# Optimization experiments

Measured on AMD Instinct MI355X. Metric: run time of the kernel, lower is better.

The kernel has to match this reference:

```python
import jax, jax.numpy as jnp
import numpy as np
import math

B, T = 8, 1024
IN_DIMS = 1024
OUT_DIMS = 1024
NUM_CODES = 1024
NUM_CODEBOOKS = 8


def setup_inputs() -> dict:
    key = jax.random.key(0)
    k1, k2, k3, k4, k5 = jax.random.split(key, 5)
    x = jax.random.normal(k1, (B, T, IN_DIMS), dtype=jnp.float32)
    target = jax.random.randint(k2, (B, T, NUM_CODEBOOKS), 0, NUM_CODES, dtype=jnp.int64)
    # params, init per reset_params()
    codebook = jax.random.normal(k3, (NUM_CODES, NUM_CODEBOOKS, OUT_DIMS), dtype=jnp.float32) / math.sqrt(OUT_DIMS * NUM_CODEBOOKS)
    proj_w = jax.random.normal(k4, (NUM_CODEBOOKS * NUM_CODES, IN_DIMS), dtype=jnp.float32) / math.sqrt(IN_DIMS)
    proj_b = jnp.zeros((NUM_CODEBOOKS * NUM_CODES,), dtype=jnp.float32)
    wproj_w = jax.random.normal(k5, (NUM_CODEBOOKS, IN_DIMS), dtype=jnp.float32) / math.sqrt(IN_DIMS)
    return {"x": x, "target": target, "codebook": codebook,
            "proj_w": proj_w, "proj_b": proj_b, "wproj_w": wproj_w}


def reference(x, target, codebook, proj_w, proj_b, wproj_w):
    # xp: (B, T, K, C)
    xp = (jnp.einsum('btd,nd->btn', x, proj_w) + proj_b).reshape(B, T, NUM_CODEBOOKS, NUM_CODES)
    # xw: (B, T, K) softmax codebook weights
    xw = jax.nn.softmax(jnp.einsum('btd,kd->btk', x, wproj_w), axis=-1)
    # gather codebook embeddings under no_grad: codebook[target, arange(K)] -> (B, T, K, D)
    cb_inds = jnp.arange(NUM_CODEBOOKS)
    codebook_embs = jax.lax.stop_gradient(codebook[target, cb_inds])
    # per-element cross entropy, reduction='none' -> (B, T, K)
    logp = jax.nn.log_softmax(xp, axis=-1)
    x_loss = -jnp.take_along_axis(logp, target[..., None], axis=-1)[..., 0]
    # softmax-weighted sum over codebooks -> (B, T, D)
    emb = jnp.einsum('btkd,btk->btd', codebook_embs, xw)
    return emb, x_loss
```

## Files before the change

kernel.cpp:

```cpp
#include <hip/hip_runtime.h>
#include <hip/hip_bf16.h>
#include <math.h>

#define MTOT   8192
#define KDIM   1024
#define NCODES 1024
#define NCB    8
#define NTOT   8192
#define ODIM   1024

typedef __attribute__((ext_vector_type(8))) short  bf16x8;
typedef __attribute__((ext_vector_type(4))) float  f32x4;

__device__ __forceinline__ ushort f2bf(float f) {
  union { float f; unsigned u; } v; v.f = f;
  unsigned u = v.u;
  unsigned r = (u + 0x7fffu + ((u >> 16) & 1u)) >> 16;
  return (ushort)r;
}

__device__ __forceinline__ void gload16(const void* g, void* l) {
  __builtin_amdgcn_global_load_lds(
      (const __attribute__((address_space(1))) void*)g,
      (__attribute__((address_space(3))) void*)l,
      16, 0, 0);
}

__global__ void cvt_bf16_kernel(const float* __restrict__ in,
                                ushort* __restrict__ out) {
  int i = blockIdx.x * blockDim.x + threadIdx.x;
  float4 v = ((const float4*)in)[i];
  ushort4 o;
  o.x = f2bf(v.x); o.y = f2bf(v.y); o.z = f2bf(v.z); o.w = f2bf(v.w);
  ((ushort4*)out)[i] = o;
}


#define SRC_DEC(c) ((((c) >> 7) * 16 + (((c) >> 3) & 15)) * 2048 \
                    + ((((c) & 7) ^ (((c) >> 3) & 7)) << 4))

#define STAGE(T) do { \
    const int kt_ = (T) & 15, ns_ = (T) >> 4, P_ = (T) & 1; \
    const char* as_ = Ag + kt_ * 128; \
    char* ad_ = ldsA_st + P_ * 32768; \
    gload16(as_ + srcA0, ad_); \
    gload16(as_ + srcA1, ad_ + 8192); \
    gload16(as_ + srcA2, ad_ + 16384); \
    gload16(as_ + srcA3, ad_ + 24576); \
    const char* bs_ = Bg + ns_ * 262144 + kt_ * 128; \
    char* bd_ = ldsB_st + P_ * 16384; \
    gload16(bs_ + srcA0, bd_); \
    gload16(bs_ + srcA1, bd_ + 8192); \
  } while(0)

#define READS(T, AR, BR) do { \
    const int P_ = (T) & 1; \
    const char* ab_ = ldsA_rd + P_ * 32768; \
    const char* bb_ = ldsB_rd + P_ * 16384; \
    _Pragma("unroll") for (int m_ = 0; m_ < 4; ++m_) { \
      AR[m_][0] = *(const bf16x8*)(ab_ + m_ * 2048 + ik0); \
      AR[m_][1] = *(const bf16x8*)(ab_ + m_ * 2048 + ik1); \
    } \
    _Pragma("unroll") for (int n_ = 0; n_ < 4; ++n_) { \
      BR[n_][0] = *(const bf16x8*)(bb_ + n_ * 2048 + ik0); \
      BR[n_][1] = *(const bf16x8*)(bb_ + n_ * 2048 + ik1); \
    } \
  } while(0)

#define MMALL(AR, BR) do { \
    _Pragma("unroll") for (int k_ = 0; k_ < 2; ++k_) \
    _Pragma("unroll") for (int m_ = 0; m_ < 4; ++m_) \
    _Pragma("unroll") for (int n_ = 0; n_ < 4; ++n_) \
      acc[m_][n_] = __builtin_amdgcn_mfma_f32_16x16x32_bf16( \
          AR[m_][k_], BR[n_][k_], acc[m_][n_], 0, 0, 0); \
  } while(0)

#define BOUNDARY \
    asm volatile("s_waitcnt lgkmcnt(0)" ::: "memory"); \
    asm volatile("s_waitcnt vmcnt(0)" ::: "memory"); \
    asm volatile("s_barrier" ::: "memory");

#define FLUSH(SEG) do { \
    const int colb_ = (SEG) * 128 + wc * 64; \
    float bias_n[4]; \
    _Pragma("unroll") for (int n_ = 0; n_ < 4; ++n_) \
      bias_n[n_] = bias[kcb * 1024 + colb_ + n_ * 16 + c15]; \
    _Pragma("unroll") for (int m_ = 0; m_ < 4; ++m_) { \
      _Pragma("unroll") for (int j_ = 0; j_ < 4; ++j_) { \
        const int rl_ = wr * 64 + m_ * 16 + g * 4 + j_; \
        const int tc_ = tgtcol[rl_]; \
        float s_ = 0.f; \
        _Pragma("unroll") for (int n_ = 0; n_ < 4; ++n_) { \
          const float v_ = acc[m_][n_][j_] + bias_n[n_]; \
          if (colb_ + n_ * 16 + c15 == tc_) tgtval[rl_] = v_; \
          s_ += __expf(v_); \
        } \
        _Pragma("unroll") for (int o_ = 1; o_ < 16; o_ <<= 1) \
          s_ += __shfl_xor(s_, o_); \
        if (c15 == 0) redS[wc * 256 + rl_] = s_; \
      } \
    } \
    asm volatile("s_waitcnt lgkmcnt(0)" ::: "memory"); \
    asm volatile("s_barrier" ::: "memory"); \
    if (tid < 256) S_acc += redS[tid] + redS[tid + 256]; \
    _Pragma("unroll") for (int m_ = 0; m_ < 4; ++m_) \
      _Pragma("unroll") for (int n_ = 0; n_ < 4; ++n_) \
        acc[m_][n_] = (f32x4){0.f, 0.f, 0.f, 0.f}; \
  } while(0)

__global__ __launch_bounds__(512, 2)
void ce_gemm_kernel(const ushort* __restrict__ Abf,
                    const ushort* __restrict__ Bbf,
                    const float*  __restrict__ bias,
                    const int*    __restrict__ target,
                    float* __restrict__ xloss) {
  extern __shared__ char smem[];
  float* redS   = (float*)(smem + 98304);
  int*   tgtcol = (int*)  (smem + 100352);
  float* tgtval = (float*)(smem + 101376);

  const int tid  = threadIdx.x;
  const int wid  = tid >> 6;
  const int lane = tid & 63;
  const int wr   = wid >> 1;
  const int wc   = wid & 1;
  const int g    = lane >> 4;
  const int c15  = lane & 15;
  const int bidx  = blockIdx.x;
  const int u     = bidx >> 3;
  const int mtile = (bidx & 7) * 4 + (u & 3);
  const int kcb   = u >> 2;

  const int ik0 = c15 * 128 + ((g ^ (c15 & 7)) << 4);
  const int ik1 = ik0 ^ 64;

  const char* ldsA_rd = smem + wr * 8192;
  const char* ldsB_rd = smem + 65536 + wc * 8192;
  char* ldsA_st = smem + wid * 1024;
  char* ldsB_st = smem + 65536 + wid * 1024;

  const char* Ag = ((const char*)Abf) + (size_t)mtile * 256 * 2048;
  const char* Bg = ((const char*)Bbf) + (size_t)kcb * 1024 * 2048;

  const int srcA0 = SRC_DEC(tid);
  const int srcA1 = SRC_DEC(tid + 512);
  const int srcA2 = SRC_DEC(tid + 1024);
  const int srcA3 = SRC_DEC(tid + 1536);

  if (tid < 256)
    tgtcol[tid] = target[(size_t)(mtile * 256 + tid) * NCB + kcb];

  f32x4 acc[4][4];
#pragma unroll
  for (int m = 0; m < 4; ++m)
#pragma unroll
    for (int n = 0; n < 4; ++n)
      acc[m][n] = (f32x4){0.f, 0.f, 0.f, 0.f};

  float S_acc = 0.f;
  bf16x8 a0[4][2], b0v[4][2], a1[4][2], b1v[4][2];

  STAGE(0); STAGE(1);
  asm volatile("s_waitcnt vmcnt(0)" ::: "memory");
  __syncthreads();
  READS(0, a0, b0v);

#pragma unroll 1
  for (int di = 0; di < 63; ++di) {
    const int t = 2 * di;
    STAGE(t + 2);
    READS(t + 1, a1, b1v);
    __builtin_amdgcn_s_setprio(1);
    MMALL(a0, b0v);
    __builtin_amdgcn_s_setprio(0);
    BOUNDARY
    STAGE(t + 3);
    READS(t + 2, a0, b0v);
    __builtin_amdgcn_s_setprio(1);
    MMALL(a1, b1v);
    __builtin_amdgcn_s_setprio(0);
    BOUNDARY
    if ((di & 7) == 7) FLUSH(di >> 3);
  }
  READS(127, a1, b1v);
  __builtin_amdgcn_s_setprio(1);
  MMALL(a0, b0v);
  __builtin_amdgcn_s_setprio(0);
  BOUNDARY
  MMALL(a1, b1v);
  FLUSH(7);

  if (tid < 256) {
    const int row = mtile * 256 + tid;
    xloss[(size_t)row * NCB + kcb] = __logf(S_acc) - tgtval[tid];
  }
}

__global__ void emb_kernel(const float* __restrict__ x,
                           const int*   __restrict__ target,
                           const float* __restrict__ cb,
                           const float* __restrict__ wproj,
                           float* __restrict__ emb_out,
                           ushort* __restrict__ xbf) {
  const int bt   = blockIdx.x;
  const int tid  = threadIdx.x;
  const int lane = tid & 63;
  const int wid  = tid >> 6;

  const float4 xv = ((const float4*)(x + (size_t)bt * KDIM))[tid];
  ushort4 xo;
  xo.x = f2bf(xv.x); xo.y = f2bf(xv.y); xo.z = f2bf(xv.z); xo.w = f2bf(xv.w);
  ((ushort4*)(xbf + (size_t)bt * KDIM))[tid] = xo;

  float p[8];
#pragma unroll
  for (int k = 0; k < 8; ++k) {
    const float4 wv = ((const float4*)(wproj + k * KDIM))[tid];
    p[k] = xv.x * wv.x + xv.y * wv.y + xv.z * wv.z + xv.w * wv.w;
  }
#pragma unroll
  for (int k = 0; k < 8; ++k)
#pragma unroll
    for (int off = 32; off >= 1; off >>= 1)
      p[k] += __shfl_xor(p[k], off);

  __shared__ float lred[4][8];
  if (lane == 0) {
#pragma unroll
    for (int k = 0; k < 8; ++k) lred[wid][k] = p[k];
  }
  __syncthreads();

  float logit[8], mx = -1e30f;
#pragma unroll
  for (int k = 0; k < 8; ++k) {
    logit[k] = lred[0][k] + lred[1][k] + lred[2][k] + lred[3][k];
    mx = fmaxf(mx, logit[k]);
  }
  float w[8], den = 0.f;
#pragma unroll
  for (int k = 0; k < 8; ++k) { w[k] = __expf(logit[k] - mx); den += w[k]; }
  const float inv = 1.f / den;

  float4 acc = make_float4(0.f, 0.f, 0.f, 0.f);
#pragma unroll
  for (int k = 0; k < 8; ++k) {
    const int t = target[bt * NCB + k];
    const float4 cv = ((const float4*)(cb + ((size_t)t * NCB + k) * ODIM))[tid];
    const float wk = w[k] * inv;
    acc.x += wk * cv.x; acc.y += wk * cv.y; acc.z += wk * cv.z; acc.w += wk * cv.w;
  }
  ((float4*)(emb_out + (size_t)bt * ODIM))[tid] = acc;
}

extern "C" void kernel_launch(void* const* d_in, const int* in_sizes, int n_in,
                              void* d_out, int out_size, void* d_ws, size_t ws_size,
                              hipStream_t stream) {
  const float* x        = (const float*)d_in[0];
  const int*   target   = (const int*)  d_in[1];
  const float* codebook = (const float*)d_in[2];
  const float* proj_w   = (const float*)d_in[3];
  const float* proj_b   = (const float*)d_in[4];
  const float* wproj_w  = (const float*)d_in[5];

  float* out       = (float*)d_out;
  float* emb_out   = out;
  float* xloss_out = out + (size_t)MTOT * ODIM;

  char* ws = (char*)d_ws;
  ushort* xbf = (ushort*)ws;
  ushort* wbf = (ushort*)(ws + (size_t)16 * 1024 * 1024);

  hipFuncSetAttribute((const void*)ce_gemm_kernel,
                      hipFuncAttributeMaxDynamicSharedMemorySize, 102400);

  emb_kernel<<<MTOT, 256, 0, stream>>>(x, target, codebook, wproj_w, emb_out, xbf);
  cvt_bf16_kernel<<<(NTOT * KDIM / 4) / 256, 256, 0, stream>>>(proj_w, wbf);

  ce_gemm_kernel<<<256, 512, 102400, stream>>>(xbf, wbf, proj_b, target, xloss_out);
}
```

Baseline: 194.0 us.

## Triple-buffer LDS staging in CE GEMM with partial vmcnt waits

Switches the bf16 GEMM's global-to-LDS staging from two buffers to three, issuing loads three k-steps ahead and waiting only on the oldest stage (vmcnt(6)) before each barrier instead of draining all loads. The main loop is restructured into six-step windows so buffer indices rotate mod 3 with compile-time register ping-pong. This aims to hide global load latency behind MFMA work, at the cost of raising dynamic LDS to about 148KB per block.

After: 207.0 us. 6.7% more time.

```diff
diff --git a/kernel.cpp b/kernel.cpp
--- a/kernel.cpp
+++ b/kernel.cpp
@@ -40,7 +40,7 @@
                     + ((((c) & 7) ^ (((c) >> 3) & 7)) << 4))
 
 #define STAGE(T) do { \
-    const int kt_ = (T) & 15, ns_ = (T) >> 4, P_ = (T) & 1; \
+    const int kt_ = (T) & 15, ns_ = (T) >> 4, P_ = (T) % 3; \
     const char* as_ = Ag + kt_ * 128; \
     char* ad_ = ldsA_st + P_ * 32768; \
     gload16(as_ + srcA0, ad_); \
@@ -54,7 +54,7 @@
   } while(0)
 
 #define READS(T, AR, BR) do { \
-    const int P_ = (T) & 1; \
+    const int P_ = (T) % 3; \
     const char* ab_ = ldsA_rd + P_ * 32768; \
     const char* bb_ = ldsB_rd + P_ * 16384; \
     _Pragma("unroll") for (int m_ = 0; m_ < 4; ++m_) { \
@@ -74,11 +74,6 @@
       acc[m_][n_] = __builtin_amdgcn_mfma_f32_16x16x32_bf16( \
           AR[m_][k_], BR[n_][k_], acc[m_][n_], 0, 0, 0); \
   } while(0)
-
-#define BOUNDARY \
-    asm volatile("s_waitcnt lgkmcnt(0)" ::: "memory"); \
-    asm volatile("s_waitcnt vmcnt(0)" ::: "memory"); \
-    asm volatile("s_barrier" ::: "memory");
 
 #define FLUSH(SEG) do { \
     const int colb_ = (SEG) * 128 + wc * 64; \
@@ -108,6 +103,19 @@
         acc[m_][n_] = (f32x4){0.f, 0.f, 0.f, 0.f}; \
   } while(0)
 
+#define WINDOW(T, CUA, CUB, SPA, SPB) do { \
+    if ((T) < 125) STAGE((T) + 3); \
+    READS((T) + 1, SPA, SPB); \
+    __builtin_amdgcn_s_setprio(1); \
+    MMALL(CUA, CUB); \
+    __builtin_amdgcn_s_setprio(0); \
+    asm volatile("s_waitcnt lgkmcnt(0)" ::: "memory"); \
+    if ((T) < 125) { asm volatile("s_waitcnt vmcnt(6)" ::: "memory"); } \
+    else           { asm volatile("s_waitcnt vmcnt(0)" ::: "memory"); } \
+    asm volatile("s_barrier" ::: "memory"); \
+    if (((T) & 15) == 15) FLUSH((T) >> 4); \
+  } while(0)
+
 __global__ __launch_bounds__(512, 2)
 void ce_gemm_kernel(const ushort* __restrict__ Abf,
                     const ushort* __restrict__ Bbf,
@@ -115,9 +123,9 @@
                     const int*    __restrict__ target,
                     float* __restrict__ xloss) {
   extern __shared__ char smem[];
-  float* redS   = (float*)(smem + 98304);
-  int*   tgtcol = (int*)  (smem + 100352);
-  float* tgtval = (float*)(smem + 101376);
+  float* redS   = (float*)(smem + 147456);
+  int*   tgtcol = (int*)  (smem + 149504);
+  float* tgtval = (float*)(smem + 150528);
 
   const int tid  = threadIdx.x;
   const int wid  = tid >> 6;
@@ -135,9 +143,9 @@
   const int ik1 = ik0 ^ 64;
 
   const char* ldsA_rd = smem + wr * 8192;
-  const char* ldsB_rd = smem + 65536 + wc * 8192;
+  const char* ldsB_rd = smem + 98304 + wc * 8192;
   char* ldsA_st = smem + wid * 1024;
-  char* ldsB_st = smem + 65536 + wid * 1024;
+  char* ldsB_st = smem + 98304 + wid * 1024;
 
   const char* Ag = ((const char*)Abf) + (size_t)mtile * 256 * 2048;
   const char* Bg = ((const char*)Bbf) + (size_t)kcb * 1024 * 2048;
@@ -160,33 +168,27 @@
   float S_acc = 0.f;
   bf16x8 a0[4][2], b0v[4][2], a1[4][2], b1v[4][2];
 
-  STAGE(0); STAGE(1);
-  asm volatile("s_waitcnt vmcnt(0)" ::: "memory");
+  STAGE(0); STAGE(1); STAGE(2);
+  asm volatile("s_waitcnt vmcnt(12)" ::: "memory");
   __syncthreads();
   READS(0, a0, b0v);
 
 #pragma unroll 1
-  for (int di = 0; di < 63; ++di) {
-    const int t = 2 * di;
-    STAGE(t + 2);
-    READS(t + 1, a1, b1v);
-    __builtin_amdgcn_s_setprio(1);
-    MMALL(a0, b0v);
-    __builtin_amdgcn_s_setprio(0);
-    BOUNDARY
-    STAGE(t + 3);
-    READS(t + 2, a0, b0v);
-    __builtin_amdgcn_s_setprio(1);
-    MMALL(a1, b1v);
-    __builtin_amdgcn_s_setprio(0);
-    BOUNDARY
-    if ((di & 7) == 7) FLUSH(di >> 3);
+  for (int bi = 0; bi < 21; ++bi) {
+    const int t0 = bi * 6;
+    WINDOW(t0 + 0, a0, b0v, a1, b1v);
+    WINDOW(t0 + 1, a1, b1v, a0, b0v);
+    WINDOW(t0 + 2, a0, b0v, a1, b1v);
+    WINDOW(t0 + 3, a1, b1v, a0, b0v);
+    WINDOW(t0 + 4, a0, b0v, a1, b1v);
+    WINDOW(t0 + 5, a1, b1v, a0, b0v);
   }
   READS(127, a1, b1v);
   __builtin_amdgcn_s_setprio(1);
   MMALL(a0, b0v);
   __builtin_amdgcn_s_setprio(0);
-  BOUNDARY
+  asm volatile("s_waitcnt lgkmcnt(0)" ::: "memory");
+  asm volatile("s_barrier" ::: "memory");
   MMALL(a1, b1v);
   FLUSH(7);
 
@@ -272,10 +274,10 @@
   ushort* wbf = (ushort*)(ws + (size_t)16 * 1024 * 1024);
 
   hipFuncSetAttribute((const void*)ce_gemm_kernel,
-                      hipFuncAttributeMaxDynamicSharedMemorySize, 102400);
+                      hipFuncAttributeMaxDynamicSharedMemorySize, 151552);
 
   emb_kernel<<<MTOT, 256, 0, stream>>>(x, target, codebook, wproj_w, emb_out, xbf);
   cvt_bf16_kernel<<<(NTOT * KDIM / 4) / 256, 256, 0, stream>>>(proj_w, wbf);
 
-  ce_gemm_kernel<<<256, 512, 102400, stream>>>(xbf, wbf, proj_b, target, xloss_out);
-}
+  ce_gemm_kernel<<<256, 512, 151552, stream>>>(xbf, wbf, proj_b, target, xloss_out);
+}
```
